# Optimization experiments

Measured on AMD Instinct MI355X. Metric: run time of the kernel, lower is better.

## Reference

```python
import jax, jax.numpy as jnp
import numpy as np

B, S, D_IN, D = 4, 4096, 512, 256


def setup_inputs() -> dict:
    key = jax.random.key(0)
    ks = jax.random.split(key, 7)
    return {
        "query": jax.random.normal(ks[0], (B, S, D_IN), dtype=jnp.float32),
        "key": jax.random.normal(ks[1], (B, S, D_IN), dtype=jnp.float32),
        "value": jax.random.normal(ks[2], (B, S, D), dtype=jnp.float32),
        "Wq": jax.random.normal(ks[3], (D, D_IN), dtype=jnp.float32) * (1.0 / np.sqrt(D_IN)),
        "bq": jax.random.normal(ks[4], (D,), dtype=jnp.float32) * 0.01,
        "Wk": jax.random.normal(ks[5], (D, D_IN), dtype=jnp.float32) * (1.0 / np.sqrt(D_IN)),
        "bk": jax.random.normal(ks[6], (D,), dtype=jnp.float32) * 0.01,
        "scale_factor": jnp.ones((), dtype=jnp.float32),  # source uses scale_factor = 1
        "dropout_p": 0,  # fixed to 0 -> dropout is identity (deterministic baseline)
    }


def reference(query, key, value, Wq, bq, Wk, bk, scale_factor, dropout_p):
    # q/k linear projections: [B,S,512] -> [B,S,256]
    q = jnp.einsum("bsi,di->bsd", query, Wq) + bq
    k = jnp.einsum("bsi,di->bsd", key, Wk) + bk
    # scaled dot-product attention scores [B,S,S]
    scores = jnp.einsum("bqd,bkd->bqk", q, k) * scale_factor
    attn = jax.nn.softmax(scores, axis=-1)
    # dropout_p == 0 -> identity
    out = jnp.einsum("bqk,bkd->bqd", attn, value)
    return out
```

## Files before the change

### kernel.cpp

```cpp
#include <hip/hip_runtime.h>

#define S_LEN 4096
#define NROWS 16384

typedef float f32x4 __attribute__((ext_vector_type(4)));
typedef _Float16 f16x8 __attribute__((ext_vector_type(8)));

__device__ __forceinline__ unsigned short f2h(float f) {
  _Float16 h = (_Float16)f;
  return __builtin_bit_cast(unsigned short, h);
}

__device__ __forceinline__ void gload16(const void* g, void* l) {
  __builtin_amdgcn_global_load_lds(
      (const __attribute__((address_space(1))) void*)g,
      (__attribute__((address_space(3))) void*)l, 16, 0, 0);
}

__global__ void cw_kernel(const float* __restrict__ Wq, const float* __restrict__ Wk,
                          unsigned short* __restrict__ Wqb, unsigned short* __restrict__ Wkb) {
  const int i = (blockIdx.x * 256 + threadIdx.x) * 8;
  if (i >= 131072) return;
  unsigned short tmp[8] __attribute__((aligned(16)));
#pragma unroll
  for (int u = 0; u < 8; ++u) tmp[u] = f2h(Wq[i + u]);
  *(uint4*)(Wqb + i) = ((const uint4*)tmp)[0];
#pragma unroll
  for (int u = 0; u < 8; ++u) tmp[u] = f2h(Wk[i + u]);
  *(uint4*)(Wkb + i) = ((const uint4*)tmp)[0];
}

__global__ __launch_bounds__(256) void vt_kernel(const float* __restrict__ V,
                                                 unsigned short* __restrict__ Vt) {
  __shared__ float tile[64][65];
  const int tid = threadIdx.x;
  const int b = blockIdx.z, s0 = blockIdx.x * 64, d0 = blockIdx.y * 64;
  {
    const int r = tid >> 2, cs = (tid & 3) * 16;
    const float* src = V + ((long)b * S_LEN + s0 + r) * 256 + d0 + cs;
#pragma unroll
    for (int u = 0; u < 4; ++u) {
      const f32x4 v = __builtin_nontemporal_load((const f32x4*)(src + 4 * u));
      tile[r][cs + 4 * u + 0] = v[0]; tile[r][cs + 4 * u + 1] = v[1];
      tile[r][cs + 4 * u + 2] = v[2]; tile[r][cs + 4 * u + 3] = v[3];
    }
  }
  __syncthreads();
  {
    const int d = tid >> 2, ss = (tid & 3) * 16;
    unsigned short tmp[16] __attribute__((aligned(16)));
#pragma unroll
    for (int u = 0; u < 16; ++u) tmp[u] = f2h(tile[ss + u][d]);
    unsigned short* dst = Vt + ((long)b * 256 + d0 + d) * S_LEN + s0 + ss;
    *(uint4*)dst = ((const uint4*)tmp)[0];
    *((uint4*)dst + 1) = ((const uint4*)tmp)[1];
  }
}

__global__ __launch_bounds__(256, 4) void proj_kernel(
    const float* __restrict__ Xq, const float* __restrict__ Xk,
    const unsigned short* __restrict__ Wqb, const unsigned short* __restrict__ Wkb,
    const float* __restrict__ bq, const float* __restrict__ bk,
    unsigned short* __restrict__ Qb, unsigned short* __restrict__ Kb,
    const float* __restrict__ scale_ptr) {
  const int tid = threadIdx.x;
  const int lane = tid & 63, w = tid >> 6;
  const int h = lane >> 4, cc = lane & 15;
  const int z = blockIdx.y;
  const float* X = z ? Xk : Xq;
  const unsigned short* Wb = z ? Wkb : Wqb;
  const float* bias = z ? bk : bq;
  unsigned short* out = z ? Kb : Qb;
  const float sc = z ? 1.f : scale_ptr[0];
  const int rowbase = blockIdx.x * 64;

  __shared__ char sx[8192];
  __shared__ char sw[32768];

  f32x4 acc[16];
  const f32x4 fz = {0.f, 0.f, 0.f, 0.f};
#pragma unroll
  for (int nf = 0; nf < 16; ++nf) acc[nf] = fz;

  for (int kstep = 0; kstep < 8; ++kstep) {
    const int k0 = kstep * 64;
    __syncthreads();
    {
      const int r = tid >> 2;
      const int cb0 = (tid & 3) * 2;
      const float* src = X + (long)(rowbase + r) * 512 + k0 + (tid & 3) * 16;
      float xv[16];
#pragma unroll
      for (int u = 0; u < 4; ++u) {
        const f32x4 v = __builtin_nontemporal_load((const f32x4*)(src + 4 * u));
        xv[4 * u + 0] = v[0]; xv[4 * u + 1] = v[1];
        xv[4 * u + 2] = v[2]; xv[4 * u + 3] = v[3];
      }
      unsigned short tmp[16] __attribute__((aligned(16)));
#pragma unroll
      for (int u = 0; u < 16; ++u) tmp[u] = f2h(xv[u]);
      *(uint4*)(sx + r * 128 + ((cb0 ^ (r & 7)) * 16)) = ((const uint4*)tmp)[0];
      *(uint4*)(sx + r * 128 + (((cb0 + 1) ^ (r & 7)) * 16)) = ((const uint4*)tmp)[1];
    }
#pragma unroll
    for (int i = 0; i < 8; ++i) {
      const int off = w * 8192 + i * 1024 + lane * 16;
      const int row = off >> 7;
      const int lcb = (lane & 7) ^ (row & 7);
      gload16(Wb + (long)row * 512 + k0 + lcb * 8, sw + w * 8192 + i * 1024);
    }
    __syncthreads();
#pragma unroll
    for (int ks = 0; ks < 2; ++ks) {
      const int rl = 16 * w + cc;
      const f16x8 af = *(const f16x8*)(sx + rl * 128 + (((h + 4 * ks) ^ (rl & 7)) * 16));
#pragma unroll
      for (int nf = 0; nf < 16; ++nf) {
        const int n = cc + 16 * nf;
        const f16x8 bf = *(const f16x8*)(sw + n * 128 + (((h + 4 * ks) ^ (n & 7)) * 16));
        acc[nf] = __builtin_amdgcn_mfma_f32_16x16x32_f16(af, bf, acc[nf], 0, 0, 0);
      }
    }
  }
#pragma unroll
  for (int nf = 0; nf < 16; ++nf) {
    const float bv = bias[cc + 16 * nf];
#pragma unroll
    for (int r = 0; r < 4; ++r) {
      const long grow = rowbase + 16 * w + 4 * h + r;
      out[grow * 256 + cc + 16 * nf] = f2h((acc[nf][r] + bv) * sc);
    }
  }
}

__global__ __launch_bounds__(512, 2) void attn_kernel(
    const unsigned short* __restrict__ Qb, const unsigned short* __restrict__ Kb,
    const unsigned short* __restrict__ Vt, float* __restrict__ out0,
    float* __restrict__ partials, float2* __restrict__ stats,
    int* __restrict__ cnt, int nsplit, int nchunks) {
  extern __shared__ char smem[];
  const int tid = threadIdx.x;
  const int lane = tid & 63, w = tid >> 6;
  const int h = lane >> 4, c = lane & 15;

  int* s_item_p = (int*)(smem + 131072);
  if (tid == 0) {
    const unsigned x = __builtin_amdgcn_s_getreg(6164) & 7u;
    const int pref = (int)x * nchunks / 8;
    int item = 0;
    for (int k = 0; k < nchunks; ++k) {
      const int ch = (pref + k) % nchunks;
      const int t = atomicAdd(cnt + ch, 1);
      if (t < 32) { item = ch * 32 + t; break; }
    }
    *s_item_p = item;
  }
  __syncthreads();
  const int nid = *s_item_p;
  const int gqt = nid & 127;
  const int split = nid >> 7;

  const int b = gqt >> 5;
  const int qrow0 = (gqt & 31) * 128;
  const long brow = (long)b * S_LEN;

  const int kv_len = S_LEN / nsplit;
  const int kv0 = split * kv_len;
  const int nit = kv_len / 64;

  f16x8 qf[8];
  {
    const unsigned short* qbase = Qb + (brow + qrow0 + w * 16 + c) * 256 + h * 8;
#pragma unroll
    for (int kk = 0; kk < 8; ++kk)
      qf[kk] = *(const f16x8*)(qbase + kk * 32);
  }

  f32x4 O[16];
  float mrun[4], lrun[4];
  const f32x4 fz = {0.f, 0.f, 0.f, 0.f};
#pragma unroll
  for (int nfd = 0; nfd < 16; ++nfd) O[nfd] = fz;
#pragma unroll
  for (int r = 0; r < 4; ++r) { mrun[r] = -1e30f; lrun[r] = 0.f; }

  const unsigned short* kbB = Kb + brow * 256;
  const unsigned short* vbB = Vt + (long)b * 256 * S_LEN;

  auto stage = [&](int buf, int it) {
    const int kvb = kv0 + it * 64;
#pragma unroll
    for (int i = 0; i < 4; ++i) {
      const int off = w * 4096 + i * 1024 + lane * 16;
      {
        const int row = off >> 9;
        const int lcb = (lane & 31) ^ (row & 7);
        gload16(kbB + (long)(kvb + row) * 256 + lcb * 8,
                smem + buf * 32768 + w * 4096 + i * 1024);
      }
      {
        const int drow = off >> 7;
        const int lcb = (lane & 7) ^ (drow & 7);
        gload16(vbB + (long)drow * S_LEN + kvb + lcb * 8,
                smem + 65536 + buf * 32768 + w * 4096 + i * 1024);
      }
    }
  };

  stage(0, 0);
  __syncthreads();

  char* const pt = smem + 131072 + w * 2048;

  for (int it = 0; it < nit; ++it) {
    const int buf = it & 1;
    if (it + 1 < nit) stage(buf ^ 1, it + 1);
    const char* kt = smem + buf * 32768;
    const char* vl = smem + 65536 + buf * 32768;

    f32x4 s[4];
#pragma unroll
    for (int nf = 0; nf < 4; ++nf) s[nf] = fz;

    __builtin_amdgcn_s_setprio(1);
#pragma unroll
    for (int kk = 0; kk < 8; ++kk) {
#pragma unroll
      for (int nf = 0; nf < 4; ++nf) {
        const int r = c + 16 * nf;
        const int cb = (4 * kk + h) ^ (r & 7);
        const f16x8 kf = *(const f16x8*)(kt + r * 512 + cb * 16);
        s[nf] = __builtin_amdgcn_mfma_f32_16x16x32_f16(qf[kk], kf, s[nf], 0, 0, 0);
      }
    }
    __builtin_amdgcn_s_setprio(0);

    {
      float lmax[4];
      bool ok = true;
#pragma unroll
      for (int r = 0; r < 4; ++r) {
        lmax[r] = fmaxf(fmaxf(s[0][r], s[1][r]), fmaxf(s[2][r], s[3][r]));
        ok &= (lmax[r] <= mrun[r] + 8.f);
      }
      if (__all(ok)) {
#pragma unroll
        for (int r = 0; r < 4; ++r) {
          float ls = 0.f;
#pragma unroll
          for (int nf = 0; nf < 4; ++nf) {
            const float p = __expf(s[nf][r] - mrun[r]);
            s[nf][r] = p; ls += p;
          }
          lrun[r] += ls;
        }
      } else {
#pragma unroll
        for (int r = 0; r < 4; ++r) {
          float mx = lmax[r];
          mx = fmaxf(mx, __shfl_xor(mx, 1));
          mx = fmaxf(mx, __shfl_xor(mx, 2));
          mx = fmaxf(mx, __shfl_xor(mx, 4));
          mx = fmaxf(mx, __shfl_xor(mx, 8));
          const float mnew = fmaxf(mrun[r], mx);
          const float alpha = __expf(mrun[r] - mnew);
          float ls = 0.f;
#pragma unroll
          for (int nf = 0; nf < 4; ++nf) {
            const float p = __expf(s[nf][r] - mnew);
            s[nf][r] = p; ls += p;
          }
          lrun[r] = lrun[r] * alpha + ls;
          mrun[r] = mnew;
#pragma unroll
          for (int nfd = 0; nfd < 16; ++nfd) O[nfd][r] *= alpha;
        }
      }
#pragma unroll
      for (int nf = 0; nf < 4; ++nf)
#pragma unroll
        for (int r = 0; r < 4; ++r) {
          const int R = 4 * h + r;
          const int C = c + 16 * nf;
          *(unsigned short*)(pt + R * 128 + (((C >> 3) ^ (R & 7)) * 16) + (C & 7) * 2) =
              f2h(s[nf][r]);
        }
    }
    asm volatile("" ::: "memory");

    __builtin_amdgcn_s_setprio(1);
#pragma unroll
    for (int ks = 0; ks < 2; ++ks) {
      const f16x8 pa = *(const f16x8*)(pt + c * 128 + (((h + 4 * ks) ^ (c & 7)) * 16));
#pragma unroll
      for (int nfd = 0; nfd < 16; ++nfd) {
        const int dr = c + 16 * nfd;
        const f16x8 vf = *(const f16x8*)(vl + dr * 128 + (((h + 4 * ks) ^ (dr & 7)) * 16));
        O[nfd] = __builtin_amdgcn_mfma_f32_16x16x32_f16(pa, vf, O[nfd], 0, 0, 0);
      }
    }
    __builtin_amdgcn_s_setprio(0);
    __syncthreads();
  }

#pragma unroll
  for (int r = 0; r < 4; ++r) {
    float l = lrun[r];
    l += __shfl_xor(l, 1); l += __shfl_xor(l, 2);
    l += __shfl_xor(l, 4); l += __shfl_xor(l, 8);
    lrun[r] = l;
  }

  const long rowg0 = brow + qrow0 + w * 16 + 4 * h;
  if (nsplit == 1) {
    float inv[4];
#pragma unroll
    for (int r = 0; r < 4; ++r) inv[r] = 1.f / lrun[r];
#pragma unroll
    for (int nfd = 0; nfd < 16; ++nfd)
#pragma unroll
      for (int r = 0; r < 4; ++r)
        out0[(rowg0 + r) * 256 + c + 16 * nfd] = O[nfd][r] * inv[r];
  } else {
    float* dst = (split == 0) ? out0 : (partials + (long)(split - 1) * NROWS * 256);
#pragma unroll
    for (int nfd = 0; nfd < 16; ++nfd)
#pragma unroll
      for (int r = 0; r < 4; ++r)
        dst[(rowg0 + r) * 256 + c + 16 * nfd] = O[nfd][r];
    if (c == 0) {
#pragma unroll
      for (int r = 0; r < 4; ++r)
        stats[(long)split * NROWS + rowg0 + r] = make_float2(mrun[r], lrun[r]);
    }
  }
}

__global__ __launch_bounds__(256) void merge_kernel(float* __restrict__ out0,
                                                    const float* __restrict__ partials,
                                                    const float2* __restrict__ stats,
                                                    int nsplit) {
  const int i4 = blockIdx.x * 256 + threadIdx.x;
  const int row = i4 >> 6;
  float2 st[4];
#pragma unroll
  for (int s = 0; s < 4; ++s)
    st[s] = (s < nsplit) ? stats[s * NROWS + row] : make_float2(-1e30f, 0.f);
  const float m = fmaxf(fmaxf(st[0].x, st[1].x), fmaxf(st[2].x, st[3].x));
  float e[4], den = 0.f;
#pragma unroll
  for (int s = 0; s < 4; ++s) { e[s] = __expf(st[s].x - m); den += st[s].y * e[s]; }
  const float invd = 1.f / den;
  float ax = 0.f, ay = 0.f, az = 0.f, aw = 0.f;
#pragma unroll
  for (int s = 0; s < 4; ++s) {
    if (s < nsplit) {
      const float* src = (s == 0) ? (const float*)out0
                                  : partials + (long)(s - 1) * NROWS * 256;
      const f32x4 v = ((const f32x4*)src)[i4];
      ax += v[0] * e[s]; ay += v[1] * e[s]; az += v[2] * e[s]; aw += v[3] * e[s];
    }
  }
  const f32x4 res = {ax * invd, ay * invd, az * invd, aw * invd};
  ((f32x4*)out0)[i4] = res;
}

extern "C" void kernel_launch(void* const* d_in, const int* in_sizes, int n_in,
                              void* d_out, int out_size, void* d_ws, size_t ws_size,
                              hipStream_t stream) {
  const float* query = (const float*)d_in[0];
  const float* key   = (const float*)d_in[1];
  const float* value = (const float*)d_in[2];
  const float* Wq    = (const float*)d_in[3];
  const float* bq    = (const float*)d_in[4];
  const float* Wk    = (const float*)d_in[5];
  const float* bk    = (const float*)d_in[6];
  const float* scale = (const float*)d_in[7];
  float* out = (float*)d_out;

  char* ws = (char*)d_ws;
  unsigned short* Wqb = (unsigned short*)(ws);
  unsigned short* Wkb = (unsigned short*)(ws + 262144);
  unsigned short* Qb  = (unsigned short*)(ws + 524288);
  unsigned short* Kb  = (unsigned short*)(ws + 8912896);
  unsigned short* Vt  = (unsigned short*)(ws + 17301504);
  int* cnt            = (int*)(ws + 25690112);
  float2* stats       = (float2*)(ws + 25694208);
  float* partials     = (float*)(ws + 26218496);

  int nsplit = 1;
  if (ws_size >= 76550144) nsplit = 4;
  else if (ws_size >= 42995712) nsplit = 2;
  const int nblk = 128 * nsplit;
  const int nchunks = nblk / 32;

  hipMemsetAsync(cnt, 0, 64, stream);
  cw_kernel<<<64, 256, 0, stream>>>(Wq, Wk, Wqb, Wkb);
  vt_kernel<<<dim3(64, 4, 4), 256, 0, stream>>>(value, Vt);
  proj_kernel<<<dim3(256, 2), 256, 0, stream>>>(query, key, Wqb, Wkb, bq, bk, Qb, Kb, scale);

  hipFuncSetAttribute((const void*)attn_kernel,
                      hipFuncAttributeMaxDynamicSharedMemorySize, 147456);
  attn_kernel<<<nblk, 512, 147456, stream>>>(Qb, Kb, Vt, out, partials,
                                             stats, cnt, nsplit, nchunks);
  if (nsplit > 1)
    merge_kernel<<<4096, 256, 0, stream>>>(out, partials, stats, nsplit);
}
```

Baseline: 200.1 us.

## Software-pipeline attention loop so QK^T of next tile overlaps PV of previous

```diff
diff --git a/kernel.cpp b/kernel.cpp
--- a/kernel.cpp
+++ b/kernel.cpp
@@ -207,21 +207,9 @@
     }
   };
 
-  stage(0, 0);
-  __syncthreads();
-
   char* const pt = smem + 131072 + w * 2048;
 
-  for (int it = 0; it < nit; ++it) {
-    const int buf = it & 1;
-    if (it + 1 < nit) stage(buf ^ 1, it + 1);
-    const char* kt = smem + buf * 32768;
-    const char* vl = smem + 65536 + buf * 32768;
-
-    f32x4 s[4];
-#pragma unroll
-    for (int nf = 0; nf < 4; ++nf) s[nf] = fz;
-
+  auto qkt = [&](const char* kt, f32x4 (&s)[4]) {
     __builtin_amdgcn_s_setprio(1);
 #pragma unroll
     for (int kk = 0; kk < 8; ++kk) {
@@ -234,60 +222,9 @@
       }
     }
     __builtin_amdgcn_s_setprio(0);
-
-    {
-      float lmax[4];
-      bool ok = true;
-#pragma unroll
-      for (int r = 0; r < 4; ++r) {
-        lmax[r] = fmaxf(fmaxf(s[0][r], s[1][r]), fmaxf(s[2][r], s[3][r]));
-        ok &= (lmax[r] <= mrun[r] + 8.f);
-      }
-      if (__all(ok)) {
-#pragma unroll
-        for (int r = 0; r < 4; ++r) {
-          float ls = 0.f;
-#pragma unroll
-          for (int nf = 0; nf < 4; ++nf) {
-            const float p = __expf(s[nf][r] - mrun[r]);
-            s[nf][r] = p; ls += p;
-          }
-          lrun[r] += ls;
-        }
-      } else {
-#pragma unroll
-        for (int r = 0; r < 4; ++r) {
-          float mx = lmax[r];
-          mx = fmaxf(mx, __shfl_xor(mx, 1));
-          mx = fmaxf(mx, __shfl_xor(mx, 2));
-          mx = fmaxf(mx, __shfl_xor(mx, 4));
-          mx = fmaxf(mx, __shfl_xor(mx, 8));
-          const float mnew = fmaxf(mrun[r], mx);
-          const float alpha = __expf(mrun[r] - mnew);
-          float ls = 0.f;
-#pragma unroll
-          for (int nf = 0; nf < 4; ++nf) {
-            const float p = __expf(s[nf][r] - mnew);
-            s[nf][r] = p; ls += p;
-          }
-          lrun[r] = lrun[r] * alpha + ls;
-          mrun[r] = mnew;
-#pragma unroll
-          for (int nfd = 0; nfd < 16; ++nfd) O[nfd][r] *= alpha;
-        }
-      }
-#pragma unroll
-      for (int nf = 0; nf < 4; ++nf)
-#pragma unroll
-        for (int r = 0; r < 4; ++r) {
-          const int R = 4 * h + r;
-          const int C = c + 16 * nf;
-          *(unsigned short*)(pt + R * 128 + (((C >> 3) ^ (R & 7)) * 16) + (C & 7) * 2) =
-              f2h(s[nf][r]);
-        }
-    }
-    asm volatile("" ::: "memory");
-
+  };
+
+  auto pv = [&](const char* vl) {
     __builtin_amdgcn_s_setprio(1);
 #pragma unroll
     for (int ks = 0; ks < 2; ++ks) {
@@ -300,8 +237,100 @@
       }
     }
     __builtin_amdgcn_s_setprio(0);
-    __syncthreads();
-  }
+  };
+
+  auto softmax_p = [&](f32x4 (&s)[4]) {
+    float lmax[4];
+    bool ok = true;
+#pragma unroll
+    for (int r = 0; r < 4; ++r) {
+      lmax[r] = fmaxf(fmaxf(s[0][r], s[1][r]), fmaxf(s[2][r], s[3][r]));
+      ok &= (lmax[r] <= mrun[r] + 8.f);
+    }
+    if (__all(ok)) {
+#pragma unroll
+      for (int r = 0; r < 4; ++r) {
+        float ls = 0.f;
+#pragma unroll
+        for (int nf = 0; nf < 4; ++nf) {
+          const float p = __expf(s[nf][r] - mrun[r]);
+          s[nf][r] = p; ls += p;
+        }
+        lrun[r] += ls;
+      }
+    } else {
+#pragma unroll
+      for (int r = 0; r < 4; ++r) {
+        float mx = lmax[r];
+        mx = fmaxf(mx, __shfl_xor(mx, 1));
+        mx = fmaxf(mx, __shfl_xor(mx, 2));
+        mx = fmaxf(mx, __shfl_xor(mx, 4));
+        mx = fmaxf(mx, __shfl_xor(mx, 8));
+        const float mnew = fmaxf(mrun[r], mx);
+        const float alpha = __expf(mrun[r] - mnew);
+        float ls = 0.f;
+#pragma unroll
+        for (int nf = 0; nf < 4; ++nf) {
+          const float p = __expf(s[nf][r] - mnew);
+          s[nf][r] = p; ls += p;
+        }
+        lrun[r] = lrun[r] * alpha + ls;
+        mrun[r] = mnew;
+#pragma unroll
+        for (int nfd = 0; nfd < 16; ++nfd) O[nfd][r] *= alpha;
+      }
+    }
+#pragma unroll
+    for (int nf = 0; nf < 4; ++nf)
+#pragma unroll
+      for (int r = 0; r < 4; ++r) {
+        const int R = 4 * h + r;
+        const int C = c + 16 * nf;
+        *(unsigned short*)(pt + R * 128 + (((C >> 3) ^ (R & 7)) * 16) + (C & 7) * 2) =
+            f2h(s[nf][r]);
+      }
+    asm volatile("" ::: "memory");
+  };
+
+  stage(0, 0);
+  __syncthreads();
+
+  {
+    f32x4 s[4];
+#pragma unroll
+    for (int nf = 0; nf < 4; ++nf) s[nf] = fz;
+    qkt(smem, s);
+    if (nit > 1) stage(1, 1);
+    softmax_p(s);
+    asm volatile("s_waitcnt vmcnt(0)" ::: "memory");
+    __builtin_amdgcn_sched_barrier(0);
+    __builtin_amdgcn_s_barrier();
+  }
+
+  for (int t = 1; t < nit; ++t) {
+    const int buf = t & 1;
+    const char* kt = smem + buf * 32768;
+    const char* vlp = smem + 65536 + (buf ^ 1) * 32768;
+
+    f32x4 s[4];
+#pragma unroll
+    for (int nf = 0; nf < 4; ++nf) s[nf] = fz;
+    qkt(kt, s);
+    pv(vlp);
+
+    asm volatile("s_waitcnt lgkmcnt(0)" ::: "memory");
+    __builtin_amdgcn_sched_barrier(0);
+    __builtin_amdgcn_s_barrier();
+
+    if (t + 1 < nit) stage(buf ^ 1, t + 1);
+    softmax_p(s);
+
+    asm volatile("s_waitcnt vmcnt(0)" ::: "memory");
+    __builtin_amdgcn_sched_barrier(0);
+    __builtin_amdgcn_s_barrier();
+  }
+
+  pv(smem + 65536 + ((nit - 1) & 1) * 32768);
 
 #pragma unroll
   for (int r = 0; r < 4; ++r) {
```

Result: no change. 198.7 us (-0.7%).
